# Kernel optimization log

Hardware: AMD Instinct MI355X
Metric: run time of the kernel (lower is better)

## Reference

```python
import jax, jax.numpy as jnp
import numpy as np

E = 30000          # nEdges
K_PER_EDGE = 12    # quadruplets per edge
KMAX = 16          # padded K dimension
Q = E * K_PER_EDGE # nQuadruplets = 360000
I = 180000         # intermediate (db) expansion size
DE, DQ, DB = 128, 64, 64   # emb_size_edge, emb_size_quad, emb_size_bilinear
DRBF, DCBF, DSBF = 16, 16, 32
NSPH = 32
SCALE_SILU = 1.0 / 0.6


def _act(x):
    # GemNet ScaledSiLU
    return jax.nn.silu(x) * SCALE_SILU


def setup_inputs() -> dict:
    key = jax.random.key(0)
    ks = jax.random.split(key, 16)
    inp = {}
    inp["m"] = jax.random.normal(ks[0], (E, DE), jnp.float32)
    inp["rbf"] = jax.random.normal(ks[1], (E, DRBF), jnp.float32)
    inp["cbf"] = jax.random.normal(ks[2], (I, DCBF), jnp.float32)
    inp["sbf_W1"] = jax.random.normal(ks[3], (E, DSBF, NSPH), jnp.float32) * 0.1
    inp["sph"] = jax.random.normal(ks[4], (E, KMAX, NSPH), jnp.float32) * 0.1
    # structured, valid scatter indices: 12 distinct K-slots per edge
    inp["Kidx4"] = jnp.tile(jnp.arange(K_PER_EDGE, dtype=jnp.int32), E)
    inp["id4_reduce_ca"] = jnp.repeat(jnp.arange(E, dtype=jnp.int32), K_PER_EDGE)
    inp["id_swap"] = jax.random.permutation(ks[5], E).astype(jnp.int32)
    inp["id4_expand_intm_db"] = jax.random.randint(ks[6], (I,), 0, E, jnp.int32)
    inp["id4_expand_abd"] = jax.random.randint(ks[7], (Q,), 0, I, jnp.int32)
    # parameters (bias-free Dense layers + bilinear weight + scaling factors)
    def w(k, shape, fan_in):
        return jax.random.normal(k, shape, jnp.float32) / np.sqrt(fan_in)
    inp["W_db"] = w(ks[8], (DE, DE), DE)
    inp["W_rbf"] = w(ks[9], (DRBF, DE), DRBF)
    inp["W_down"] = w(ks[10], (DE, DQ), DE)
    inp["W_cbf"] = w(ks[11], (DCBF, DQ), DCBF)
    inp["W_bilin"] = w(ks[12], (DQ, DSBF, DB), DQ * DSBF)
    inp["W_up_ca"] = w(ks[13], (DB, DE), DB)
    inp["W_up_ac"] = w(ks[14], (DB, DE), DB)
    inp["s_rbf"] = jnp.asarray(1.1, jnp.float32)
    inp["s_cbf"] = jnp.asarray(0.9, jnp.float32)
    inp["s_sbf"] = jnp.asarray(1.2, jnp.float32)
    return inp


def reference(m, rbf, cbf, sbf_W1, sph,
              W_db, W_rbf, W_down, W_cbf, W_bilin, W_up_ca, W_up_ac,
              s_rbf, s_cbf, s_sbf,
              Kidx4, id_swap, id4_reduce_ca, id4_expand_intm_db, id4_expand_abd):
    # dense_db + hadamard with rbf MLP + scale
    x_db = _act(m @ W_db)                        # (E, DE)
    x_db = (x_db * (rbf @ W_rbf)) * s_rbf        # scale_rbf scales the product
    # down projection to quad size, expand to intermediate set
    x_db = _act(x_db @ W_down)                   # (E, DQ)
    x_db = x_db[id4_expand_intm_db]              # (I, DQ)
    # hadamard with cbf MLP + scale, expand to quadruplets
    x_db = (x_db * (cbf @ W_cbf)) * s_cbf        # (I, DQ)
    x_db = x_db[id4_expand_abd]                  # (Q, DQ)
    # EfficientInteractionBilinear: scatter quads into padded (E, Kmax, DQ)
    m2 = jnp.zeros((E, KMAX, DQ), x_db.dtype).at[id4_reduce_ca, Kidx4].set(x_db)
    sum_k = jnp.einsum("eks,ekq->esq", sph, m2)          # (E, NSPH, DQ)
    rw = jnp.einsum("eis,esq->eiq", sbf_W1, sum_k)       # (E, DSBF, DQ)
    x = jnp.einsum("eiq,qib->eb", rw, W_bilin)           # (E, DB)
    x = x * s_sbf                                         # scale_sbf_sum
    # up projections; swap directions for ac
    x_ca = _act(x @ W_up_ca)                     # (E, DE)
    x_ac = _act(x @ W_up_ac)[id_swap]            # (E, DE)
    return (x_ca + x_ac) * (1.0 / np.sqrt(2.0))
```

## Files before the change

### kernel.cpp

```cpp
#include <hip/hip_runtime.h>
#include <hip/hip_bf16.h>


#define E_N   30000
#define KPE   12
#define KMAXX 16
#define I_N   180000
#define DE    128
#define DQ    64
#define DB    64
#define DRBF  16
#define DCBF  16
#define DSBF  32
#define NSPH  32
#define SCALE_SILU (1.0f/0.6f)
#define INV_SQRT2  0.70710678118654752f

typedef __attribute__((ext_vector_type(8))) short bf16x8;
typedef __attribute__((ext_vector_type(4))) float f32x4;

__device__ __forceinline__ float silu_scaled(float x) {
    return x / (1.0f + __expf(-x)) * SCALE_SILU;
}

__device__ __forceinline__ short f2bf(float x) {
    unsigned u = __float_as_uint(x);
    u += 0x7fffu + ((u >> 16) & 1u);
    return (short)(u >> 16);
}

__device__ __forceinline__ bf16x8 cvt8(const float4 a, const float4 b) {
    bf16x8 t;
    t[0]=f2bf(a.x); t[1]=f2bf(a.y); t[2]=f2bf(a.z); t[3]=f2bf(a.w);
    t[4]=f2bf(b.x); t[5]=f2bf(b.y); t[6]=f2bf(b.z); t[7]=f2bf(b.w);
    return t;
}

#define PK_WDBT   0
#define PK_WRBFT  16384
#define PK_WDOWNT 20480
#define PK_WUPAT  28672
#define PK_WUPBT  36864
#define PK_BT     45056
#define PK_TOTAL  176128

__global__ __launch_bounds__(256) void kw_prep(
    const float* __restrict__ Wdb, const float* __restrict__ Wrbf,
    const float* __restrict__ Wdown, const float* __restrict__ WupA,
    const float* __restrict__ WupB, const float* __restrict__ Wbil,
    ushort* __restrict__ wpk)
{
    const int idx = blockIdx.x * 256 + threadIdx.x;
    float v;
    if (idx < PK_WRBFT) {
        const int n = idx >> 7, k = idx & 127;
        v = Wdb[k * DE + n];
    } else if (idx < PK_WDOWNT) {
        const int j = idx - PK_WRBFT;
        const int n = j >> 5, k = j & 31;
        v = (k < DRBF) ? Wrbf[k * DE + n] : 0.f;
    } else if (idx < PK_WUPAT) {
        const int j = idx - PK_WDOWNT;
        const int q = j >> 7, k = j & 127;
        v = Wdown[k * DQ + q];
    } else if (idx < PK_WUPBT) {
        const int j = idx - PK_WUPAT;
        const int d = j >> 6, b = j & 63;
        v = WupA[b * DE + d];
    } else if (idx < PK_BT) {
        const int j = idx - PK_WUPBT;
        const int d = j >> 6, b = j & 63;
        v = WupB[b * DE + d];
    } else {
        const int j = idx - PK_BT;
        const int b = j >> 11, jj = j & 2047;
        const int i = jj >> 6, q = jj & 63;
        v = Wbil[(size_t)(q * DSBF + i) * DB + b];
    }
    wpk[idx] = (ushort)f2bf(v);
}

__global__ __launch_bounds__(256) void k1_mfma(
    const float* __restrict__ m, const float* __restrict__ rbf,
    const ushort* __restrict__ wpk, const float* __restrict__ s_rbf_p,
    ushort* __restrict__ Tb)
{
    const int l  = threadIdx.x & 63;
    const int wv = __builtin_amdgcn_readfirstlane(threadIdx.x >> 6);
    const int e0 = (blockIdx.x * 4 + wv) * 16;
    if (e0 >= E_N) return;
    const int mr = l & 15;
    const int kg = l >> 4;
    const ushort* WdbT  = wpk + PK_WDBT;
    const ushort* WrbfT = wpk + PK_WRBFT;

    f32x4 accH[8], accR[8];
    #pragma unroll
    for (int nt = 0; nt < 8; ++nt)
        #pragma unroll
        for (int r = 0; r < 4; ++r) { accH[nt][r] = 0.f; accR[nt][r] = 0.f; }

    bf16x8 ra;
    if (kg < 2) {
        const float* rr = rbf + (size_t)(e0 + mr) * DRBF + kg * 8;
        ra = cvt8(*(const float4*)rr, *(const float4*)(rr + 4));
    } else {
        #pragma unroll
        for (int j = 0; j < 8; ++j) ra[j] = 0;
    }
    #pragma unroll
    for (int nt = 0; nt < 8; ++nt) {
        const bf16x8 rb = *(const bf16x8*)(WrbfT + (nt*16 + mr)*32 + kg*8);
        accR[nt] = __builtin_amdgcn_mfma_f32_16x16x32_bf16(ra, rb, accR[nt], 0,0,0);
    }

    const float* mrow = m + (size_t)(e0 + mr) * DE + kg * 8;
    #pragma unroll
    for (int kt = 0; kt < 4; ++kt) {
        const float* ms = mrow + kt * 32;
        const bf16x8 a = cvt8(*(const float4*)ms, *(const float4*)(ms + 4));
        #pragma unroll
        for (int nt = 0; nt < 8; ++nt) {
            const bf16x8 b = *(const bf16x8*)(WdbT + (nt*16 + mr)*128 + kt*32 + kg*8);
            accH[nt] = __builtin_amdgcn_mfma_f32_16x16x32_bf16(a, b, accH[nt], 0,0,0);
        }
    }

    const float srbf = s_rbf_p[0];
    ushort* tout = Tb + (size_t)(e0 + kg*4) * DE + mr;
    #pragma unroll
    for (int nt = 0; nt < 8; ++nt)
        #pragma unroll
        for (int r = 0; r < 4; ++r)
            tout[(size_t)r * DE + 16*nt] =
                (ushort)f2bf(silu_scaled(accH[nt][r]) * accR[nt][r] * srbf);
}

__global__ __launch_bounds__(256) void k1b_mfma(
    const ushort* __restrict__ Tb, const ushort* __restrict__ wpk,
    float* __restrict__ xq)
{
    const int l  = threadIdx.x & 63;
    const int wv = __builtin_amdgcn_readfirstlane(threadIdx.x >> 6);
    const int e0 = (blockIdx.x * 4 + wv) * 16;
    if (e0 >= E_N) return;
    const int mr = l & 15;
    const int kg = l >> 4;
    const ushort* WdownT = wpk + PK_WDOWNT;

    f32x4 acc[4];
    #pragma unroll
    for (int nt = 0; nt < 4; ++nt)
        #pragma unroll
        for (int r = 0; r < 4; ++r) acc[nt][r] = 0.f;

    const ushort* arow = Tb + (size_t)(e0 + mr) * DE + kg * 8;
    #pragma unroll
    for (int kt = 0; kt < 4; ++kt) {
        const bf16x8 a = *(const bf16x8*)(arow + kt * 32);
        #pragma unroll
        for (int nt = 0; nt < 4; ++nt) {
            const bf16x8 b = *(const bf16x8*)(WdownT + (nt*16 + mr)*128 + kt*32 + kg*8);
            acc[nt] = __builtin_amdgcn_mfma_f32_16x16x32_bf16(a, b, acc[nt], 0,0,0);
        }
    }
    float* xout = xq + (size_t)(e0 + kg*4) * DQ + mr;
    #pragma unroll
    for (int nt = 0; nt < 4; ++nt)
        #pragma unroll
        for (int r = 0; r < 4; ++r)
            xout[(size_t)r * DQ + 16*nt] = silu_scaled(acc[nt][r]);
}

__global__ __launch_bounds__(256) void k2_intm(
    const float* __restrict__ cbf, const int* __restrict__ idx_db,
    const float* __restrict__ xq, const float* __restrict__ Wcbf,
    const float* __restrict__ s_cbf_p, float* __restrict__ y)
{
    __shared__ float sW[DCBF*DQ];
    for (int i = threadIdx.x; i < DCBF*DQ; i += 256) sW[i] = Wcbf[i];
    __syncthreads();
    const float sc = s_cbf_p[0];
    const int lane = threadIdx.x & 63;
    const int wv = __builtin_amdgcn_readfirstlane(threadIdx.x >> 6);
    for (int row = blockIdx.x*4 + wv; row < I_N; row += gridDim.x*4) {
        const float* cr = cbf + (size_t)row*DCBF;
        float acc = 0.f;
        #pragma unroll
        for (int k = 0; k < DCBF; ++k) acc += cr[k] * sW[k*DQ + lane];
        const int src = idx_db[row];
        y[(size_t)row*DQ + lane] = xq[(size_t)src*DQ + lane] * acc * sc;
    }
}

__global__ __launch_bounds__(256) void k3_fused(
    const float* __restrict__ y, const float* __restrict__ sph,
    const float* __restrict__ sbf, const int* __restrict__ kidx,
    const int* __restrict__ abd, const ushort* __restrict__ wpk,
    const float* __restrict__ s_sbf_p, ushort* __restrict__ Xb)
{
    __shared__ ushort sRw[16 * 2048];
    const int l  = threadIdx.x & 63;
    const int wv = __builtin_amdgcn_readfirstlane(threadIdx.x >> 6);
    const int e0 = blockIdx.x * 16;
    const int q0 = l & 15;
    const int sg = l >> 4;
    const int s0 = sg * 8;

    for (int ei = 0; ei < 4; ++ei) {
        const int eL = wv * 4 + ei;
        const int e  = e0 + eL;

        float SK[8][4];
        #pragma unroll
        for (int r = 0; r < 8; ++r)
            #pragma unroll
            for (int c = 0; c < 4; ++c) SK[r][c] = 0.f;

        const int base = e * KPE;
        #pragma unroll
        for (int j = 0; j < KPE; ++j) {
            const int kj = kidx[base + j];
            const int aj = abd[base + j];
            const float* yr = y + (size_t)aj * DQ;
            const float v0 = yr[q0];
            const float v1 = yr[q0 + 16];
            const float v2 = yr[q0 + 32];
            const float v3 = yr[q0 + 48];
            const float* sp = sph + ((size_t)e * KMAXX + kj) * NSPH + s0;
            const float4 sA = *(const float4*)sp;
            const float4 sB = *(const float4*)(sp + 4);
            const float sv[8] = {sA.x, sA.y, sA.z, sA.w, sB.x, sB.y, sB.z, sB.w};
            #pragma unroll
            for (int r = 0; r < 8; ++r) {
                SK[r][0] = __builtin_fmaf(sv[r], v0, SK[r][0]);
                SK[r][1] = __builtin_fmaf(sv[r], v1, SK[r][1]);
                SK[r][2] = __builtin_fmaf(sv[r], v2, SK[r][2]);
                SK[r][3] = __builtin_fmaf(sv[r], v3, SK[r][3]);
            }
        }

        bf16x8 bfrag[4];
        #pragma unroll
        for (int qt = 0; qt < 4; ++qt) {
            bf16x8 t;
            #pragma unroll
            for (int r = 0; r < 8; ++r) t[r] = f2bf(SK[r][qt]);
            bfrag[qt] = t;
        }

        const float* sb0 = sbf + ((size_t)e * DSBF + q0) * NSPH + s0;
        bf16x8 afrag[2];
        #pragma unroll
        for (int h = 0; h < 2; ++h) {
            const float* ar = sb0 + h * 16 * NSPH;
            afrag[h] = cvt8(*(const float4*)ar, *(const float4*)(ar + 4));
        }

        f32x4 acc[2][4];
        #pragma unroll
        for (int h = 0; h < 2; ++h)
            #pragma unroll
            for (int qt = 0; qt < 4; ++qt)
                #pragma unroll
                for (int r = 0; r < 4; ++r) acc[h][qt][r] = 0.f;

        #pragma unroll
        for (int h = 0; h < 2; ++h)
            #pragma unroll
            for (int qt = 0; qt < 4; ++qt)
                acc[h][qt] = __builtin_amdgcn_mfma_f32_16x16x32_bf16(
                    afrag[h], bfrag[qt], acc[h][qt], 0, 0, 0);

        ushort* ro = sRw + eL * 2048;
        const int swz = (eL & 7) << 3;
        #pragma unroll
        for (int h = 0; h < 2; ++h)
            #pragma unroll
            for (int r = 0; r < 4; ++r) {
                const int i = h * 16 + sg * 4 + r;
                #pragma unroll
                for (int qt = 0; qt < 4; ++qt)
                    ro[(i * DQ + q0 + 16 * qt) ^ swz] =
                        (ushort)f2bf(acc[h][qt][r]);
            }
    }
    __syncthreads();

    const int eA  = l & 15;
    const int kg  = l >> 4;
    const int swzA = (eA & 7) << 3;
    const ushort* brow = wpk + PK_BT + (size_t)(wv * 16 + (l & 15)) * 2048 + kg * 8;

    f32x4 xacc;
    #pragma unroll
    for (int r = 0; r < 4; ++r) xacc[r] = 0.f;

    #pragma unroll 8
    for (int kt = 0; kt < 64; ++kt) {
        const bf16x8 a = *(const bf16x8*)(sRw + eA * 2048 +
                                          ((kt * 32 + kg * 8) ^ swzA));
        const bf16x8 b = *(const bf16x8*)(brow + kt * 32);
        xacc = __builtin_amdgcn_mfma_f32_16x16x32_bf16(a, b, xacc, 0, 0, 0);
    }

    const float ss = s_sbf_p[0];
    ushort* xout = Xb + (size_t)(e0 + kg * 4) * DQ + wv * 16 + (l & 15);
    #pragma unroll
    for (int r = 0; r < 4; ++r)
        xout[(size_t)r * DQ] = (ushort)f2bf(xacc[r] * ss);
}

__global__ __launch_bounds__(256) void k4_mfma(
    const ushort* __restrict__ Xb, const ushort* __restrict__ wpk,
    float* __restrict__ Ab, float* __restrict__ Bb)
{
    const int l  = threadIdx.x & 63;
    const int wv = __builtin_amdgcn_readfirstlane(threadIdx.x >> 6);
    const int e0 = (blockIdx.x * 4 + wv) * 16;
    if (e0 >= E_N) return;
    const int mr = l & 15;
    const int kg = l >> 4;
    const ushort* WupAT = wpk + PK_WUPAT;
    const ushort* WupBT = wpk + PK_WUPBT;

    f32x4 accA[8], accB[8];
    #pragma unroll
    for (int nt = 0; nt < 8; ++nt)
        #pragma unroll
        for (int r = 0; r < 4; ++r) { accA[nt][r] = 0.f; accB[nt][r] = 0.f; }

    const ushort* arow = Xb + (size_t)(e0 + mr) * DQ + kg * 8;
    #pragma unroll
    for (int kt = 0; kt < 2; ++kt) {
        const bf16x8 a = *(const bf16x8*)(arow + kt * 32);
        #pragma unroll
        for (int nt = 0; nt < 8; ++nt) {
            const bf16x8 bA = *(const bf16x8*)(WupAT + (nt*16 + mr)*64 + kt*32 + kg*8);
            accA[nt] = __builtin_amdgcn_mfma_f32_16x16x32_bf16(a, bA, accA[nt], 0,0,0);
            const bf16x8 bB = *(const bf16x8*)(WupBT + (nt*16 + mr)*64 + kt*32 + kg*8);
            accB[nt] = __builtin_amdgcn_mfma_f32_16x16x32_bf16(a, bB, accB[nt], 0,0,0);
        }
    }
    float* aout = Ab + (size_t)(e0 + kg*4) * DE + mr;
    float* bout = Bb + (size_t)(e0 + kg*4) * DE + mr;
    #pragma unroll
    for (int nt = 0; nt < 8; ++nt)
        #pragma unroll
        for (int r = 0; r < 4; ++r) {
            aout[(size_t)r * DE + 16*nt] = silu_scaled(accA[nt][r]);
            bout[(size_t)r * DE + 16*nt] = silu_scaled(accB[nt][r]);
        }
}

__global__ __launch_bounds__(256) void k5_comb(
    const float* __restrict__ Ab, const float* __restrict__ Bb,
    const int* __restrict__ swp, float* __restrict__ out)
{
    const int i4   = blockIdx.x*256 + threadIdx.x;
    const int flat = i4*4;
    const int e = flat >> 7;
    const int d = flat & 127;
    const float4 a = *(const float4*)(Ab + flat);
    const int es = swp[e];
    const float4 b = *(const float4*)(Bb + (size_t)es*DE + d);
    float4 o = make_float4((a.x+b.x)*INV_SQRT2, (a.y+b.y)*INV_SQRT2,
                           (a.z+b.z)*INV_SQRT2, (a.w+b.w)*INV_SQRT2);
    *(float4*)(out + flat) = o;
}

extern "C" void kernel_launch(void* const* d_in, const int* in_sizes, int n_in,
                              void* d_out, int out_size, void* d_ws, size_t ws_size,
                              hipStream_t stream)
{
    const float* m      = (const float*)d_in[0];
    const float* rbf    = (const float*)d_in[1];
    const float* cbf    = (const float*)d_in[2];
    const float* sbfW1  = (const float*)d_in[3];
    const float* sph    = (const float*)d_in[4];
    const int*   kidx   = (const int*)d_in[5];
    const int*   idswap = (const int*)d_in[7];
    const int*   idin   = (const int*)d_in[8];
    const int*   abd    = (const int*)d_in[9];
    const float* Wdb    = (const float*)d_in[10];
    const float* Wrbf   = (const float*)d_in[11];
    const float* Wdown  = (const float*)d_in[12];
    const float* Wcbf   = (const float*)d_in[13];
    const float* Wbil   = (const float*)d_in[14];
    const float* WupA   = (const float*)d_in[15];
    const float* WupB   = (const float*)d_in[16];
    const float* s_rbf  = (const float*)d_in[17];
    const float* s_cbf  = (const float*)d_in[18];
    const float* s_sbf  = (const float*)d_in[19];
    float* out = (float*)d_out;

    float* ws  = (float*)d_ws;
    ushort* Tb = (ushort*)ws;
    float* xq  = ws +  1920000;
    float* y   = ws +  3840000;
    ushort* Xb = (ushort*)(ws + 15360000);
    float* Ab  = ws + 16320000;
    float* Bb  = ws + 20160000;
    ushort* wpk= (ushort*)(ws + 24000000);

    kw_prep  <<<688,  256, 0, stream>>>(Wdb, Wrbf, Wdown, WupA, WupB, Wbil, wpk);
    k1_mfma  <<<469,  256, 0, stream>>>(m, rbf, wpk, s_rbf, Tb);
    k1b_mfma <<<469,  256, 0, stream>>>(Tb, wpk, xq);
    k2_intm  <<<1024, 256, 0, stream>>>(cbf, idin, xq, Wcbf, s_cbf, y);
    k3_fused <<<1875, 256, 0, stream>>>(y, sph, sbfW1, kidx, abd, wpk, s_sbf, Xb);
    k4_mfma  <<<469,  256, 0, stream>>>(Xb, wpk, Ab, Bb);
    k5_comb  <<<3750, 256, 0, stream>>>(Ab, Bb, idswap, out);
}
```

Baseline: 472.6 us.

## Store intermediates in bf16 and halve k3 block tile to 8 edges

The intermediate y (I×DQ) and the up-projection outputs A/B become bf16 instead of fp32, halving their write and gather traffic in k2, k3, k4 and k5. k3 now handles 8 edges per block with half the LDS, a new XOR swizzle and an occupancy hint of 4, so more blocks can be resident. In the final MFMA half the lanes produce redundant rows that are discarded, and the extra bf16 rounding adds numerical error.

```diff
diff --git a/kernel.cpp b/kernel.cpp
--- a/kernel.cpp
+++ b/kernel.cpp
@@ -27,6 +27,9 @@
     unsigned u = __float_as_uint(x);
     u += 0x7fffu + ((u >> 16) & 1u);
     return (short)(u >> 16);
+}
+__device__ __forceinline__ float bf2f(ushort u) {
+    return __uint_as_float(((unsigned)u) << 16);
 }
 
 __device__ __forceinline__ bf16x8 cvt8(const float4 a, const float4 b) {
@@ -175,7 +178,7 @@
 __global__ __launch_bounds__(256) void k2_intm(
     const float* __restrict__ cbf, const int* __restrict__ idx_db,
     const float* __restrict__ xq, const float* __restrict__ Wcbf,
-    const float* __restrict__ s_cbf_p, float* __restrict__ y)
+    const float* __restrict__ s_cbf_p, ushort* __restrict__ y)
 {
     __shared__ float sW[DCBF*DQ];
     for (int i = threadIdx.x; i < DCBF*DQ; i += 256) sW[i] = Wcbf[i];
@@ -189,26 +192,27 @@
         #pragma unroll
         for (int k = 0; k < DCBF; ++k) acc += cr[k] * sW[k*DQ + lane];
         const int src = idx_db[row];
-        y[(size_t)row*DQ + lane] = xq[(size_t)src*DQ + lane] * acc * sc;
-    }
-}
-
-__global__ __launch_bounds__(256) void k3_fused(
-    const float* __restrict__ y, const float* __restrict__ sph,
+        y[(size_t)row*DQ + lane] =
+            (ushort)f2bf(xq[(size_t)src*DQ + lane] * acc * sc);
+    }
+}
+
+__global__ __launch_bounds__(256, 4) void k3_fused(
+    const ushort* __restrict__ y, const float* __restrict__ sph,
     const float* __restrict__ sbf, const int* __restrict__ kidx,
     const int* __restrict__ abd, const ushort* __restrict__ wpk,
     const float* __restrict__ s_sbf_p, ushort* __restrict__ Xb)
 {
-    __shared__ ushort sRw[16 * 2048];
+    __shared__ ushort sRw[8 * 2048];
     const int l  = threadIdx.x & 63;
     const int wv = __builtin_amdgcn_readfirstlane(threadIdx.x >> 6);
-    const int e0 = blockIdx.x * 16;
+    const int e0 = blockIdx.x * 8;
     const int q0 = l & 15;
     const int sg = l >> 4;
     const int s0 = sg * 8;
 
-    for (int ei = 0; ei < 4; ++ei) {
-        const int eL = wv * 4 + ei;
+    for (int ei = 0; ei < 2; ++ei) {
+        const int eL = wv * 2 + ei;
         const int e  = e0 + eL;
 
         float SK[8][4];
@@ -222,11 +226,11 @@
         for (int j = 0; j < KPE; ++j) {
             const int kj = kidx[base + j];
             const int aj = abd[base + j];
-            const float* yr = y + (size_t)aj * DQ;
-            const float v0 = yr[q0];
-            const float v1 = yr[q0 + 16];
-            const float v2 = yr[q0 + 32];
-            const float v3 = yr[q0 + 48];
+            const ushort* yr = y + (size_t)aj * DQ;
+            const float v0 = bf2f(yr[q0]);
+            const float v1 = bf2f(yr[q0 + 16]);
+            const float v2 = bf2f(yr[q0 + 32]);
+            const float v3 = bf2f(yr[q0 + 48]);
             const float* sp = sph + ((size_t)e * KMAXX + kj) * NSPH + s0;
             const float4 sA = *(const float4*)sp;
             const float4 sB = *(const float4*)(sp + 4);
@@ -273,24 +277,24 @@
                     afrag[h], bfrag[qt], acc[h][qt], 0, 0, 0);
 
         ushort* ro = sRw + eL * 2048;
-        const int swz = (eL & 7) << 3;
         #pragma unroll
         for (int h = 0; h < 2; ++h)
             #pragma unroll
             for (int r = 0; r < 4; ++r) {
                 const int i = h * 16 + sg * 4 + r;
                 #pragma unroll
-                for (int qt = 0; qt < 4; ++qt)
-                    ro[(i * DQ + q0 + 16 * qt) ^ swz] =
-                        (ushort)f2bf(acc[h][qt][r]);
+                for (int qt = 0; qt < 4; ++qt) {
+                    const int f = i * DQ + q0 + 16 * qt;
+                    ro[f ^ (sg << 4) ^ (eL << 3)] = (ushort)f2bf(acc[h][qt][r]);
+                }
             }
     }
     __syncthreads();
 
-    const int eA  = l & 15;
+    const int eA  = l & 7;
     const int kg  = l >> 4;
-    const int swzA = (eA & 7) << 3;
     const ushort* brow = wpk + PK_BT + (size_t)(wv * 16 + (l & 15)) * 2048 + kg * 8;
+    const ushort* arow = sRw + eA * 2048;
 
     f32x4 xacc;
     #pragma unroll
@@ -298,22 +302,25 @@
 
     #pragma unroll 8
     for (int kt = 0; kt < 64; ++kt) {
-        const bf16x8 a = *(const bf16x8*)(sRw + eA * 2048 +
-                                          ((kt * 32 + kg * 8) ^ swzA));
+        const int f0 = kt * 32 + kg * 8;
+        const int S0 = f0 ^ ((((unsigned)kt >> 3) & 3) << 4) ^ (eA << 3);
+        const bf16x8 a = *(const bf16x8*)(arow + S0);
         const bf16x8 b = *(const bf16x8*)(brow + kt * 32);
         xacc = __builtin_amdgcn_mfma_f32_16x16x32_bf16(a, b, xacc, 0, 0, 0);
     }
 
     const float ss = s_sbf_p[0];
-    ushort* xout = Xb + (size_t)(e0 + kg * 4) * DQ + wv * 16 + (l & 15);
-    #pragma unroll
-    for (int r = 0; r < 4; ++r)
-        xout[(size_t)r * DQ] = (ushort)f2bf(xacc[r] * ss);
+    if (sg < 2) {
+        ushort* xout = Xb + (size_t)(e0 + sg * 4) * DQ + wv * 16 + (l & 15);
+        #pragma unroll
+        for (int r = 0; r < 4; ++r)
+            xout[(size_t)r * DQ] = (ushort)f2bf(xacc[r] * ss);
+    }
 }
 
 __global__ __launch_bounds__(256) void k4_mfma(
     const ushort* __restrict__ Xb, const ushort* __restrict__ wpk,
-    float* __restrict__ Ab, float* __restrict__ Bb)
+    ushort* __restrict__ Abh, ushort* __restrict__ Bbh)
 {
     const int l  = threadIdx.x & 63;
     const int wv = __builtin_amdgcn_readfirstlane(threadIdx.x >> 6);
@@ -342,31 +349,39 @@
             accB[nt] = __builtin_amdgcn_mfma_f32_16x16x32_bf16(a, bB, accB[nt], 0,0,0);
         }
     }
-    float* aout = Ab + (size_t)(e0 + kg*4) * DE + mr;
-    float* bout = Bb + (size_t)(e0 + kg*4) * DE + mr;
+    ushort* aout = Abh + (size_t)(e0 + kg*4) * DE + mr;
+    ushort* bout = Bbh + (size_t)(e0 + kg*4) * DE + mr;
     #pragma unroll
     for (int nt = 0; nt < 8; ++nt)
         #pragma unroll
         for (int r = 0; r < 4; ++r) {
-            aout[(size_t)r * DE + 16*nt] = silu_scaled(accA[nt][r]);
-            bout[(size_t)r * DE + 16*nt] = silu_scaled(accB[nt][r]);
+            aout[(size_t)r * DE + 16*nt] = (ushort)f2bf(silu_scaled(accA[nt][r]));
+            bout[(size_t)r * DE + 16*nt] = (ushort)f2bf(silu_scaled(accB[nt][r]));
         }
 }
 
 __global__ __launch_bounds__(256) void k5_comb(
-    const float* __restrict__ Ab, const float* __restrict__ Bb,
+    const ushort* __restrict__ Abh, const ushort* __restrict__ Bbh,
     const int* __restrict__ swp, float* __restrict__ out)
 {
-    const int i4   = blockIdx.x*256 + threadIdx.x;
-    const int flat = i4*4;
+    const int i8   = blockIdx.x*256 + threadIdx.x;
+    const int flat = i8*8;
     const int e = flat >> 7;
     const int d = flat & 127;
-    const float4 a = *(const float4*)(Ab + flat);
+    const bf16x8 a = *(const bf16x8*)(Abh + flat);
     const int es = swp[e];
-    const float4 b = *(const float4*)(Bb + (size_t)es*DE + d);
-    float4 o = make_float4((a.x+b.x)*INV_SQRT2, (a.y+b.y)*INV_SQRT2,
-                           (a.z+b.z)*INV_SQRT2, (a.w+b.w)*INV_SQRT2);
-    *(float4*)(out + flat) = o;
+    const bf16x8 b = *(const bf16x8*)(Bbh + (size_t)es*DE + d);
+    float4 o0, o1;
+    o0.x = (bf2f((ushort)a[0]) + bf2f((ushort)b[0])) * INV_SQRT2;
+    o0.y = (bf2f((ushort)a[1]) + bf2f((ushort)b[1])) * INV_SQRT2;
+    o0.z = (bf2f((ushort)a[2]) + bf2f((ushort)b[2])) * INV_SQRT2;
+    o0.w = (bf2f((ushort)a[3]) + bf2f((ushort)b[3])) * INV_SQRT2;
+    o1.x = (bf2f((ushort)a[4]) + bf2f((ushort)b[4])) * INV_SQRT2;
+    o1.y = (bf2f((ushort)a[5]) + bf2f((ushort)b[5])) * INV_SQRT2;
+    o1.z = (bf2f((ushort)a[6]) + bf2f((ushort)b[6])) * INV_SQRT2;
+    o1.w = (bf2f((ushort)a[7]) + bf2f((ushort)b[7])) * INV_SQRT2;
+    *(float4*)(out + flat)     = o0;
+    *(float4*)(out + flat + 4) = o1;
 }
 
 extern "C" void kernel_launch(void* const* d_in, const int* in_sizes, int n_in,
@@ -394,20 +409,20 @@
     const float* s_sbf  = (const float*)d_in[19];
     float* out = (float*)d_out;
 
-    float* ws  = (float*)d_ws;
-    ushort* Tb = (ushort*)ws;
-    float* xq  = ws +  1920000;
-    float* y   = ws +  3840000;
-    ushort* Xb = (ushort*)(ws + 15360000);
-    float* Ab  = ws + 16320000;
-    float* Bb  = ws + 20160000;
-    ushort* wpk= (ushort*)(ws + 24000000);
+    float* ws   = (float*)d_ws;
+    ushort* Tb  = (ushort*)ws;
+    float*  xq  = ws +  1920000;
+    ushort* y   = (ushort*)(ws + 3840000);
+    ushort* Xb  = (ushort*)(ws + 9600000);
+    ushort* Abh = (ushort*)(ws + 10560000);
+    ushort* Bbh = (ushort*)(ws + 12480000);
+    ushort* wpk = (ushort*)(ws + 14400000);
 
     kw_prep  <<<688,  256, 0, stream>>>(Wdb, Wrbf, Wdown, WupA, WupB, Wbil, wpk);
     k1_mfma  <<<469,  256, 0, stream>>>(m, rbf, wpk, s_rbf, Tb);
     k1b_mfma <<<469,  256, 0, stream>>>(Tb, wpk, xq);
     k2_intm  <<<1024, 256, 0, stream>>>(cbf, idin, xq, Wcbf, s_cbf, y);
-    k3_fused <<<1875, 256, 0, stream>>>(y, sph, sbfW1, kidx, abd, wpk, s_sbf, Xb);
-    k4_mfma  <<<469,  256, 0, stream>>>(Xb, wpk, Ab, Bb);
-    k5_comb  <<<3750, 256, 0, stream>>>(Ab, Bb, idswap, out);
-}
+    k3_fused <<<3750, 256, 0, stream>>>(y, sph, sbfW1, kidx, abd, wpk, s_sbf, Xb);
+    k4_mfma  <<<469,  256, 0, stream>>>(Xb, wpk, Abh, Bbh);
+    k5_comb  <<<1875, 256, 0, stream>>>(Abh, Bbh, idswap, out);
+}
```

New measurement: 517.4 us. 1.09x slower.
